# Kernel optimization log

Measured on AMD Instinct MI355X. Metric: run time of the kernel, lower is better.

## Reference

```python
import jax, jax.numpy as jnp
import numpy as np

ALPHA = 1.0

def setup_inputs() -> dict:
    key = jax.random.key(0)
    k1, k2 = jax.random.split(key)
    B, T, F = 8, 4096, 1024
    x = jax.random.normal(k1, (B, T, F), dtype=jnp.float32)
    # ragged valid lengths in [T//2, T]; mask[b, t] = t < length[b]
    lengths = jax.random.randint(k2, (B,), T // 2, T + 1)
    attention_mask = (jnp.arange(T)[None, :] < lengths[:, None]).astype(jnp.int32)
    return {"input_values": x, "attention_mask": attention_mask}


def reference(input_values, attention_mask):
    # input_values: [B,T,F]; attention_mask: [B,T] (1 for valid, 0 for pad)
    m = attention_mask.astype(input_values.dtype)[..., None]          # [B,T,1]
    L = jnp.sum(m, axis=1)                                            # [B,1]
    # k: per-channel mean over valid timesteps (torch mean over dims [-1,-2])
    k = jnp.sum(input_values * m, axis=1) / L                         # [B,F]
    k_centered = k - jnp.mean(k, axis=-1, keepdims=True)              # [B,F] (center over channels)
    kd = jnp.sqrt(jnp.sum(k_centered ** 2, axis=-1, keepdims=True))   # [B,1]
    # center each timestep over channels
    x_centered = input_values - jnp.mean(input_values, axis=-1, keepdims=True)  # [B,T,F]
    qd = jnp.sqrt(jnp.sum(x_centered ** 2, axis=-1))                  # [B,T]
    num = jnp.einsum('btf,bf->bt', x_centered, k_centered)            # [B,T]
    C_qk = num / (qd * kd)                                            # [B,T]
    A = (1.0 - jax.nn.sigmoid(C_qk)) ** ALPHA                         # [B,T]
    # apply attention and zero out padded positions (original zero-pads)
    out = input_values * A[..., None] * m                             # [B,T,F]
    return out
```

## Files before the change

kernel.cpp:

```cpp
#include <hip/hip_runtime.h>
#include <math.h>

#define BB 8
#define TT 4096
#define FF 1024
#define F4 (FF / 4)
#define TS 64
#define TCHUNK (TT / TS)

__global__ __launch_bounds__(256) void k1_partial(const float4* __restrict__ x4,
                                                  const int* __restrict__ mask,
                                                  float4* __restrict__ part4) {
    int ts  = blockIdx.x;
    int b   = blockIdx.y;
    int tid = threadIdx.x;

    __shared__ float msh[TCHUNK];
    if (tid < TCHUNK) msh[tid] = (float)mask[(size_t)b * TT + (size_t)ts * TCHUNK + tid];
    __syncthreads();

    const float4* xb = x4 + ((size_t)b * TT + (size_t)ts * TCHUNK) * F4 + tid;
    float4 acc = make_float4(0.f, 0.f, 0.f, 0.f);
    #pragma unroll 8
    for (int t = 0; t < TCHUNK; ++t) {
        float4 v = xb[(size_t)t * F4];
        float  m = msh[t];
        acc.x = fmaf(m, v.x, acc.x);
        acc.y = fmaf(m, v.y, acc.y);
        acc.z = fmaf(m, v.z, acc.z);
        acc.w = fmaf(m, v.w, acc.w);
    }
    part4[((size_t)b * TS + ts) * F4 + tid] = acc;
}

__global__ __launch_bounds__(1024) void k2_stats(const float* __restrict__ part,
                                                 const int* __restrict__ mask,
                                                 float* __restrict__ kc,
                                                 float* __restrict__ kd_arr,
                                                 float* __restrict__ skc_arr) {
    __shared__ float redA[16];
    __shared__ float redB[16];
    __shared__ float Lsh, meansh;

    int b    = blockIdx.x;
    int tid  = threadIdx.x;
    int wave = tid >> 6;
    int lane = tid & 63;

    int cnt = 0;
    #pragma unroll
    for (int i = 0; i < 4; ++i) cnt += mask[(size_t)b * TT + tid + i * 1024];
    float fc = (float)cnt;
    #pragma unroll
    for (int off = 32; off; off >>= 1) fc += __shfl_xor(fc, off);
    if (lane == 0) redA[wave] = fc;
    __syncthreads();
    if (tid == 0) {
        float s = 0.f;
        for (int i = 0; i < 16; ++i) s += redA[i];
        Lsh = s;
    }
    __syncthreads();
    float L = Lsh;

    float s = 0.f;
    #pragma unroll 8
    for (int ts = 0; ts < TS; ++ts) s += part[((size_t)b * TS + ts) * FF + tid];
    float k = s / L;

    float m = k;
    #pragma unroll
    for (int off = 32; off; off >>= 1) m += __shfl_xor(m, off);
    __syncthreads();
    if (lane == 0) redA[wave] = m;
    __syncthreads();
    if (tid == 0) {
        float t = 0.f;
        for (int i = 0; i < 16; ++i) t += redA[i];
        meansh = t * (1.0f / FF);
    }
    __syncthreads();
    float kcv = k - meansh;
    kc[(size_t)b * FF + tid] = kcv;

    float a  = kcv * kcv;
    float c2 = kcv;
    #pragma unroll
    for (int off = 32; off; off >>= 1) {
        a  += __shfl_xor(a, off);
        c2 += __shfl_xor(c2, off);
    }
    __syncthreads();
    if (lane == 0) { redA[wave] = a; redB[wave] = c2; }
    __syncthreads();
    if (tid == 0) {
        float sa = 0.f, sc = 0.f;
        for (int i = 0; i < 16; ++i) { sa += redA[i]; sc += redB[i]; }
        kd_arr[b]  = sqrtf(sa);
        skc_arr[b] = sc;
    }
}

__global__ __launch_bounds__(256) void k3_apply(const float4* __restrict__ x4,
                                                const int* __restrict__ mask,
                                                const float4* __restrict__ kc4,
                                                const float* __restrict__ kd_arr,
                                                const float* __restrict__ skc_arr,
                                                float4* __restrict__ out4) {
    int t   = blockIdx.x;
    int b   = blockIdx.y;
    int tid = threadIdx.x;
    size_t row = ((size_t)b * TT + t) * F4;

    if (mask[(size_t)b * TT + t] == 0) {
        out4[row + tid] = make_float4(0.f, 0.f, 0.f, 0.f);
        return;
    }

    float4 xv = x4[row + tid];
    float4 kv = kc4[(size_t)b * F4 + tid];

    float s1 = xv.x + xv.y + xv.z + xv.w;
    float s2 = xv.x * xv.x + xv.y * xv.y + xv.z * xv.z + xv.w * xv.w;
    float s3 = xv.x * kv.x + xv.y * kv.y + xv.z * kv.z + xv.w * kv.w;
    #pragma unroll
    for (int off = 32; off; off >>= 1) {
        s1 += __shfl_xor(s1, off);
        s2 += __shfl_xor(s2, off);
        s3 += __shfl_xor(s3, off);
    }

    __shared__ float r1[4], r2[4], r3[4];
    int wave = tid >> 6, lane = tid & 63;
    if (lane == 0) { r1[wave] = s1; r2[wave] = s2; r3[wave] = s3; }
    __syncthreads();

    float S1 = r1[0] + r1[1] + r1[2] + r1[3];
    float S2 = r2[0] + r2[1] + r2[2] + r2[3];
    float S3 = r3[0] + r3[1] + r3[2] + r3[3];
    float mean = S1 * (1.0f / FF);
    float num  = S3 - mean * skc_arr[b];
    float qd2  = S2 - S1 * S1 * (1.0f / FF);
    float qd   = sqrtf(fmaxf(qd2, 0.f));
    float C    = num / (qd * kd_arr[b]);
    float A    = 1.0f / (1.0f + __expf(C));

    float4 o;
    o.x = xv.x * A; o.y = xv.y * A; o.z = xv.z * A; o.w = xv.w * A;
    out4[row + tid] = o;
}

extern "C" void kernel_launch(void* const* d_in, const int* in_sizes, int n_in,
                              void* d_out, int out_size, void* d_ws, size_t ws_size,
                              hipStream_t stream) {
    const float* x    = (const float*)d_in[0];
    const int*   mask = (const int*)d_in[1];
    float*       out  = (float*)d_out;

    float* part = (float*)d_ws;
    float* kc   = part + (size_t)BB * TS * FF;
    float* kd   = kc + (size_t)BB * FF;
    float* skc  = kd + BB;

    k1_partial<<<dim3(TS, BB), 256, 0, stream>>>((const float4*)x, mask, (float4*)part);
    k2_stats<<<BB, 1024, 0, stream>>>(part, mask, kc, kd, skc);
    k3_apply<<<dim3(TT, BB), 256, 0, stream>>>((const float4*)x, mask, (const float4*)kc,
                                               kd, skc, (float4*)out);
}
```

Baseline: 254.4 us.

## Map one wavefront per row in apply kernel with nontemporal stores

The apply kernel now assigns each 64-lane wavefront a full 1024-float row, so each block covers four rows. This removes the shared-memory cross-wave reduction and the block barrier. Output writes use nontemporal stores to avoid polluting cache with streamed output. The partial-sum kernel's time split doubles to 128 chunks for more parallelism in the first pass, at the cost of more partial data for the stats kernel to read.

New measurement: 254.2 us. No clear change (-0.1%).

```diff
diff --git a/kernel.cpp b/kernel.cpp
--- a/kernel.cpp
+++ b/kernel.cpp
@@ -5,8 +5,10 @@
 #define TT 4096
 #define FF 1024
 #define F4 (FF / 4)
-#define TS 64
+#define TS 128
 #define TCHUNK (TT / TS)
+
+typedef float vfloat4 __attribute__((ext_vector_type(4)));
 
 __global__ __launch_bounds__(256) void k1_partial(const float4* __restrict__ x4,
                                                   const int* __restrict__ mask,
@@ -107,22 +109,39 @@
                                                 const float* __restrict__ kd_arr,
                                                 const float* __restrict__ skc_arr,
                                                 float4* __restrict__ out4) {
-    int t   = blockIdx.x;
-    int b   = blockIdx.y;
-    int tid = threadIdx.x;
+    int wave = threadIdx.x >> 6;
+    int lane = threadIdx.x & 63;
+    int t    = blockIdx.x * 4 + wave;
+    int b    = blockIdx.y;
     size_t row = ((size_t)b * TT + t) * F4;
 
+    vfloat4* orow = (vfloat4*)(out4 + row);
     if (mask[(size_t)b * TT + t] == 0) {
-        out4[row + tid] = make_float4(0.f, 0.f, 0.f, 0.f);
+        vfloat4 z = (vfloat4)(0.f);
+        #pragma unroll
+        for (int j = 0; j < 4; ++j)
+            __builtin_nontemporal_store(z, orow + lane + 64 * j);
         return;
     }
 
-    float4 xv = x4[row + tid];
-    float4 kv = kc4[(size_t)b * F4 + tid];
+    const float4* xrow = x4 + row;
+    const float4* krow = kc4 + (size_t)b * F4;
+    float4 xv[4], kv[4];
+    #pragma unroll
+    for (int j = 0; j < 4; ++j) {
+        xv[j] = xrow[lane + 64 * j];
+        kv[j] = krow[lane + 64 * j];
+    }
 
-    float s1 = xv.x + xv.y + xv.z + xv.w;
-    float s2 = xv.x * xv.x + xv.y * xv.y + xv.z * xv.z + xv.w * xv.w;
-    float s3 = xv.x * kv.x + xv.y * kv.y + xv.z * kv.z + xv.w * kv.w;
+    float s1 = 0.f, s2 = 0.f, s3 = 0.f;
+    #pragma unroll
+    for (int j = 0; j < 4; ++j) {
+        s1 += xv[j].x + xv[j].y + xv[j].z + xv[j].w;
+        s2 = fmaf(xv[j].x, xv[j].x, fmaf(xv[j].y, xv[j].y,
+             fmaf(xv[j].z, xv[j].z, fmaf(xv[j].w, xv[j].w, s2))));
+        s3 = fmaf(xv[j].x, kv[j].x, fmaf(xv[j].y, kv[j].y,
+             fmaf(xv[j].z, kv[j].z, fmaf(xv[j].w, kv[j].w, s3))));
+    }
     #pragma unroll
     for (int off = 32; off; off >>= 1) {
         s1 += __shfl_xor(s1, off);
@@ -130,24 +149,20 @@
         s3 += __shfl_xor(s3, off);
     }
 
-    __shared__ float r1[4], r2[4], r3[4];
-    int wave = tid >> 6, lane = tid & 63;
-    if (lane == 0) { r1[wave] = s1; r2[wave] = s2; r3[wave] = s3; }
-    __syncthreads();
-
-    float S1 = r1[0] + r1[1] + r1[2] + r1[3];
-    float S2 = r2[0] + r2[1] + r2[2] + r2[3];
-    float S3 = r3[0] + r3[1] + r3[2] + r3[3];
-    float mean = S1 * (1.0f / FF);
-    float num  = S3 - mean * skc_arr[b];
-    float qd2  = S2 - S1 * S1 * (1.0f / FF);
+    float mean = s1 * (1.0f / FF);
+    float num  = s3 - mean * skc_arr[b];
+    float qd2  = s2 - s1 * s1 * (1.0f / FF);
     float qd   = sqrtf(fmaxf(qd2, 0.f));
     float C    = num / (qd * kd_arr[b]);
     float A    = 1.0f / (1.0f + __expf(C));
 
-    float4 o;
-    o.x = xv.x * A; o.y = xv.y * A; o.z = xv.z * A; o.w = xv.w * A;
-    out4[row + tid] = o;
+    #pragma unroll
+    for (int j = 0; j < 4; ++j) {
+        vfloat4 o;
+        o.x = xv[j].x * A; o.y = xv[j].y * A;
+        o.z = xv[j].z * A; o.w = xv[j].w * A;
+        __builtin_nontemporal_store(o, orow + lane + 64 * j);
+    }
 }
 
 extern "C" void kernel_launch(void* const* d_in, const int* in_sizes, int n_in,
@@ -164,6 +179,6 @@
 
     k1_partial<<<dim3(TS, BB), 256, 0, stream>>>((const float4*)x, mask, (float4*)part);
     k2_stats<<<BB, 1024, 0, stream>>>(part, mask, kc, kd, skc);
-    k3_apply<<<dim3(TT, BB), 256, 0, stream>>>((const float4*)x, mask, (const float4*)kc,
-                                               kd, skc, (float4*)out);
+    k3_apply<<<dim3(TT / 4, BB), 256, 0, stream>>>((const float4*)x, mask, (const float4*)kc,
+                                                   kd, skc, (float4*)out);
 }
```
